# Performance work log

Measured on AMD Instinct MI355X. Metric: run time of the kernel, lower is better.

## Reference

```python
import jax, jax.numpy as jnp
import numpy as np

B, A, HR = 2, 180, 512
H_OUT = W_OUT = 512


def setup_inputs() -> dict:
    key = jax.random.key(0)
    k1, = jax.random.split(key, 1)
    sino = jax.random.normal(k1, (B, A, HR), dtype=jnp.float32)
    angles_deg = jnp.linspace(0.0, 180.0, A, endpoint=False, dtype=jnp.float32)
    return {"sino": sino, "angles_deg": angles_deg, "H": H_OUT, "W": W_OUT}


def _forward(sino, angles_deg, H, W):
    Bn, An, Hr = sino.shape
    pad = int(1.0 * 0.1 * min(H, W))  # pad_ratio = 1.0
    Hp, Wp = H + 2 * pad, W + 2 * pad

    # --- F.interpolate bilinear, align_corners=False: (A,B,Hr,1) -> (A,B,Hp,Wp).
    # Input width is 1, so width interp replicates the single column; only height interp matters.
    src = jnp.clip((jnp.arange(Hp, dtype=jnp.float32) + 0.5) * (Hr / Hp) - 0.5, 0.0, Hr - 1)
    i0 = jnp.floor(src).astype(jnp.int32)
    i1 = jnp.minimum(i0 + 1, Hr - 1)
    wH = src - i0.astype(jnp.float32)
    p = jnp.transpose(sino, (1, 0, 2)).astype(jnp.float32)  # (A,B,Hr)
    col = p[:, :, i0] * (1.0 - wH) + p[:, :, i1] * wH       # (A,B,Hp)
    proj = jnp.broadcast_to(col[:, :, :, None], (An, Bn, Hp, Wp))  # (A,B,Hp,Wp)

    # --- affine_grid (align_corners=False), sign = -1
    th = -jnp.deg2rad(angles_deg)
    c, s = jnp.cos(th), jnp.sin(th)                          # (A,)
    xs = (jnp.arange(Wp, dtype=jnp.float32) + 0.5) * (2.0 / Wp) - 1.0
    ys = (jnp.arange(Hp, dtype=jnp.float32) + 0.5) * (2.0 / Hp) - 1.0
    gx = c[:, None, None] * xs[None, None, :] - s[:, None, None] * ys[None, :, None]  # (A,Hp,Wp)
    gy = s[:, None, None] * xs[None, None, :] + c[:, None, None] * ys[None, :, None]

    # --- grid_sample bilinear, zeros padding, align_corners=False
    ix = ((gx + 1.0) * Wp - 1.0) * 0.5
    iy = ((gy + 1.0) * Hp - 1.0) * 0.5
    x0 = jnp.floor(ix).astype(jnp.int32); x1 = x0 + 1
    y0 = jnp.floor(iy).astype(jnp.int32); y1 = y0 + 1
    wx = ix - x0.astype(jnp.float32)
    wy = iy - y0.astype(jnp.float32)

    def corner(img, xi, yi, w):  # img (B,Hp,Wp); idx/w (Hp,Wp)
        valid = (xi >= 0) & (xi <= Wp - 1) & (yi >= 0) & (yi <= Hp - 1)
        xc = jnp.clip(xi, 0, Wp - 1)
        yc = jnp.clip(yi, 0, Hp - 1)
        return img[:, yc, xc] * (w * valid.astype(jnp.float32))[None]

    def sample(img, x0a, x1a, y0a, y1a, wxa, wya):
        return (corner(img, x0a, y0a, (1 - wxa) * (1 - wya)) +
                corner(img, x1a, y0a, wxa * (1 - wya)) +
                corner(img, x0a, y1a, (1 - wxa) * wya) +
                corner(img, x1a, y1a, wxa * wya))

    xr = jax.vmap(sample)(proj, x0, x1, y0, y1, wx, wy)      # (A,B,Hp,Wp)
    acc = xr.sum(axis=0) / (An + 1e-06)                      # (B,Hp,Wp)
    acc = acc[:, None, :, :]                                 # (B,1,Hp,Wp)
    if pad > 0:
        acc = acc[:, :, pad:Hp - pad, pad:Wp - pad]
    return acc


def reference(sino, angles_deg, H, W):
    return _forward(sino, angles_deg, H, W)
```

## Files before the change

kernel.cpp:

```cpp
#include <hip/hip_runtime.h>
#include <math.h>

#define B_N   2
#define A_N   180
#define HR_N  512
#define H_OUT 512
#define W_OUT 512
#define PAD   51
#define HP    614
#define WP    614
#define GUARD 80
#define HPP   (HP + 2*GUARD)
#define NPIX  (H_OUT * W_OUT)

#define TILE   16
#define CH     30
#define NCH    (A_N / CH)
#define WIN    24


__device__ __forceinline__ float col_val(const float* __restrict__ sino,
                                         int b, int a, int yy) {
    if (yy < 0 || yy >= HP) return 0.0f;
    float src = ((float)yy + 0.5f) * ((float)HR_N / (float)HP) - 0.5f;
    src = fminf(fmaxf(src, 0.0f), (float)(HR_N - 1));
    int i0 = (int)floorf(src);
    int i1 = min(i0 + 1, HR_N - 1);
    float wH = src - (float)i0;
    const float* srow = sino + ((size_t)b * A_N + a) * HR_N;
    return srow[i0] * (1.0f - wH) + srow[i1] * wH;
}

__global__ void prep_kernel(const float* __restrict__ sino,
                            const float* __restrict__ angles,
                            float4* __restrict__ pk,
                            float* __restrict__ tg) {
    int idx = blockIdx.x * blockDim.x + threadIdx.x;
    if (idx < A_N) {
        float th = -angles[idx] * (float)(M_PI / 180.0);
        tg[2 * idx]     = cosf(th);
        tg[2 * idx + 1] = sinf(th);
    }
    const int total = A_N * HPP;
    if (idx < total) {
        int y = idx % HPP;
        int a = idx / HPP;
        int yy = y - GUARD;
        float4 v;
        v.x = col_val(sino, 0, a, yy);
        v.y = col_val(sino, 1, a, yy);
        v.z = col_val(sino, 0, a, yy + 1);
        v.w = col_val(sino, 1, a, yy + 1);
        pk[idx] = v;
    }
}

__global__ __launch_bounds__(256) void bp_kernel(const float4* __restrict__ pk,
                                                 const float* __restrict__ tg,
                                                 float* __restrict__ out) {
    __shared__ float4 s_ang[A_N];
    __shared__ int    s_base[A_N];
    __shared__ float4 s_win[CH * WIN];

    int t  = threadIdx.x;
    int tx = blockIdx.x, ty = blockIdx.y;

    if (t < A_N) {
        float c = tg[2 * t];
        float s = tg[2 * t + 1];
        float Xc = (float)(tx * TILE) - 248.0f;
        float Yc = (float)(ty * TILE) - 248.0f;
        float iyc = fmaf(s, Xc, fmaf(c, Yc, 306.5f));
        int base = (int)floorf(iyc) - 11;
        s_ang[t]  = make_float4(c, s, (float)base, 0.0f);
        s_base[t] = base;
    }

    int lx = t & (TILE - 1);
    int ly = t >> 4;
    int w = tx * TILE + lx;
    int h = ty * TILE + ly;
    float X = (float)w - 255.5f;
    float Y = (float)h - 255.5f;

    float acc0 = 0.0f, acc1 = 0.0f;
    __syncthreads();

    for (int ch = 0; ch < NCH; ++ch) {
        int a0 = ch * CH;
        for (int e = t; e < CH * WIN; e += 256) {
            int la = e / WIN;
            int j  = e - la * WIN;
            int a  = a0 + la;
            int yy = s_base[a] + j + GUARD;
            s_win[e] = pk[(size_t)a * HPP + yy];
        }
        __syncthreads();

#pragma unroll 6
        for (int la = 0; la < CH; ++la) {
            float4 ang = s_ang[a0 + la];
            float c = ang.x, s = ang.y, fb = ang.z;
            float ix = fmaf(c, X, fmaf(-s, Y, 306.5f));
            float iy = fmaf(s, X, fmaf(c, Y, 306.5f));

            float xfac = fminf(fmaxf(ix + 1.0f, 0.0f), 1.0f)
                       * fminf(fmaxf((float)WP - ix, 0.0f), 1.0f);

            float f  = iy - fb;
            int   li = (int)f;
            float wy = f - (float)li;

            float4 cv = s_win[la * WIN + li];
            acc0 = fmaf(xfac, fmaf(wy, cv.z - cv.x, cv.x), acc0);
            acc1 = fmaf(xfac, fmaf(wy, cv.w - cv.y, cv.y), acc1);
        }
        __syncthreads();
    }

    const float inv = 1.0f / (180.0f + 1e-6f);
    int idx = h * W_OUT + w;
    out[idx]        = acc0 * inv;
    out[NPIX + idx] = acc1 * inv;
}

extern "C" void kernel_launch(void* const* d_in, const int* in_sizes, int n_in,
                              void* d_out, int out_size, void* d_ws, size_t ws_size,
                              hipStream_t stream) {
    const float* sino   = (const float*)d_in[0];
    const float* angles = (const float*)d_in[1];
    float* ws   = (float*)d_ws;
    float4* pk  = (float4*)ws;
    float* tg   = ws + (size_t)4 * A_N * HPP;

    const int total = A_N * HPP;
    prep_kernel<<<(total + 255) / 256, 256, 0, stream>>>(sino, angles, pk, tg);

    dim3 grid(W_OUT / TILE, H_OUT / TILE);
    bp_kernel<<<grid, 256, 0, stream>>>(pk, tg, (float*)d_out);
}
```

Before: 87.25 us.

## Pack projection table as fp16 and specialize interior tiles without x-bounds masking

Measured after the change: 91.38 us. 4.7% more time.

```diff
diff --git a/kernel.cpp b/kernel.cpp
--- a/kernel.cpp
+++ b/kernel.cpp
@@ -1,4 +1,5 @@
 #include <hip/hip_runtime.h>
+#include <hip/hip_fp16.h>
 #include <math.h>
 
 #define B_N   2
@@ -13,10 +14,10 @@
 #define HPP   (HP + 2*GUARD)
 #define NPIX  (H_OUT * W_OUT)
 
-#define TILE   16
-#define CH     30
-#define NCH    (A_N / CH)
-#define WIN    24
+#define TILE  16
+#define CH    30
+#define NCH   (A_N / CH)
+#define WIN   24
 
 
 __device__ __forceinline__ float col_val(const float* __restrict__ sino,
@@ -33,93 +34,115 @@
 
 __global__ void prep_kernel(const float* __restrict__ sino,
                             const float* __restrict__ angles,
-                            float4* __restrict__ pk,
-                            float* __restrict__ tg) {
+                            uint2* __restrict__ pk2,
+                            float2* __restrict__ tg) {
     int idx = blockIdx.x * blockDim.x + threadIdx.x;
     if (idx < A_N) {
         float th = -angles[idx] * (float)(M_PI / 180.0);
-        tg[2 * idx]     = cosf(th);
-        tg[2 * idx + 1] = sinf(th);
+        tg[idx] = make_float2(cosf(th), sinf(th));
     }
     const int total = A_N * HPP;
     if (idx < total) {
         int y = idx % HPP;
         int a = idx / HPP;
         int yy = y - GUARD;
-        float4 v;
-        v.x = col_val(sino, 0, a, yy);
-        v.y = col_val(sino, 1, a, yy);
-        v.z = col_val(sino, 0, a, yy + 1);
-        v.w = col_val(sino, 1, a, yy + 1);
-        pk[idx] = v;
+        float v00 = col_val(sino, 0, a, yy);
+        float v10 = col_val(sino, 1, a, yy);
+        float v01 = col_val(sino, 0, a, yy + 1);
+        float v11 = col_val(sino, 1, a, yy + 1);
+        __half2 lo = __floats2half2_rn(v00, v10);
+        __half2 hi = __floats2half2_rn(v01, v11);
+        uint2 u;
+        u.x = *(unsigned int*)&lo;
+        u.y = *(unsigned int*)&hi;
+        pk2[idx] = u;
     }
 }
 
-__global__ __launch_bounds__(256) void bp_kernel(const float4* __restrict__ pk,
-                                                 const float* __restrict__ tg,
-                                                 float* __restrict__ out) {
-    __shared__ float4 s_ang[A_N];
-    __shared__ int    s_base[A_N];
-    __shared__ float4 s_win[CH * WIN];
-
-    int t  = threadIdx.x;
-    int tx = blockIdx.x, ty = blockIdx.y;
-
-    if (t < A_N) {
-        float c = tg[2 * t];
-        float s = tg[2 * t + 1];
-        float Xc = (float)(tx * TILE) - 248.0f;
-        float Yc = (float)(ty * TILE) - 248.0f;
-        float iyc = fmaf(s, Xc, fmaf(c, Yc, 306.5f));
-        int base = (int)floorf(iyc) - 11;
-        s_ang[t]  = make_float4(c, s, (float)base, 0.0f);
-        s_base[t] = base;
-    }
-
-    int lx = t & (TILE - 1);
-    int ly = t >> 4;
-    int w = tx * TILE + lx;
-    int h = ty * TILE + ly;
-    float X = (float)w - 255.5f;
-    float Y = (float)h - 255.5f;
-
-    float acc0 = 0.0f, acc1 = 0.0f;
-    __syncthreads();
-
+template <bool INTERIOR>
+__device__ __forceinline__ void bp_body(const uint2* __restrict__ pk2,
+                                        const float2* __restrict__ tgv,
+                                        uint2* __restrict__ s_win,
+                                        const int* __restrict__ s_base,
+                                        int t, float X, float Y, float Xc, float Yc,
+                                        float& acc0, float& acc1) {
     for (int ch = 0; ch < NCH; ++ch) {
         int a0 = ch * CH;
         for (int e = t; e < CH * WIN; e += 256) {
             int la = e / WIN;
             int j  = e - la * WIN;
             int a  = a0 + la;
-            int yy = s_base[a] + j + GUARD;
-            s_win[e] = pk[(size_t)a * HPP + yy];
+            s_win[e] = pk2[(size_t)a * HPP + (GUARD + s_base[a] + j)];
         }
         __syncthreads();
 
 #pragma unroll 6
         for (int la = 0; la < CH; ++la) {
-            float4 ang = s_ang[a0 + la];
-            float c = ang.x, s = ang.y, fb = ang.z;
-            float ix = fmaf(c, X, fmaf(-s, Y, 306.5f));
-            float iy = fmaf(s, X, fmaf(c, Y, 306.5f));
-
-            float xfac = fminf(fmaxf(ix + 1.0f, 0.0f), 1.0f)
-                       * fminf(fmaxf((float)WP - ix, 0.0f), 1.0f);
-
-            float f  = iy - fb;
+            float2 cs = tgv[a0 + la];
+            float c = cs.x, s = cs.y;
+            float iyc   = fmaf(s, Xc, fmaf(c, Yc, 306.5f));
+            float basef = floorf(iyc);
+            float iyp   = fmaf(s, X, fmaf(c, Y, 317.5f));
+            float f  = iyp - basef;
             int   li = (int)f;
             float wy = f - (float)li;
 
-            float4 cv = s_win[la * WIN + li];
-            acc0 = fmaf(xfac, fmaf(wy, cv.z - cv.x, cv.x), acc0);
-            acc1 = fmaf(xfac, fmaf(wy, cv.w - cv.y, cv.y), acc1);
+            uint2 cv = s_win[la * WIN + li];
+            __half2 lo = *(__half2*)&cv.x;
+            __half2 hi = *(__half2*)&cv.y;
+            float c00 = __low2float(lo), c10 = __high2float(lo);
+            float c01 = __low2float(hi), c11 = __high2float(hi);
+
+            if (INTERIOR) {
+                acc0 = fmaf(wy, c01 - c00, acc0 + c00);
+                acc1 = fmaf(wy, c11 - c10, acc1 + c10);
+            } else {
+                float ix = fmaf(c, X, fmaf(-s, Y, 306.5f));
+                float xf = fminf(fmaxf(ix + 1.0f, 0.0f), 1.0f)
+                         * fminf(fmaxf((float)WP - ix, 0.0f), 1.0f);
+                float t0 = fmaf(wy, c01 - c00, c00);
+                float t1 = fmaf(wy, c11 - c10, c10);
+                acc0 = fmaf(xf, t0, acc0);
+                acc1 = fmaf(xf, t1, acc1);
+            }
         }
         __syncthreads();
     }
+}
+
+__global__ __launch_bounds__(256) void bp_kernel(const uint2* __restrict__ pk2,
+                                                 const float2* __restrict__ tgv,
+                                                 float* __restrict__ out) {
+    __shared__ uint2 s_win[CH * WIN];
+    __shared__ int   s_base[A_N];
+
+    int t  = threadIdx.x;
+    int tx = blockIdx.x, ty = blockIdx.y;
+    float Xc = (float)(tx * TILE) - 248.0f;
+    float Yc = (float)(ty * TILE) - 248.0f;
+
+    if (t < A_N) {
+        float2 cs = tgv[t];
+        float iyc = fmaf(cs.y, Xc, fmaf(cs.x, Yc, 306.5f));
+        s_base[t] = (int)floorf(iyc) - 11;
+    }
+
+    int lx = t & (TILE - 1);
+    int ly = t >> 4;
+    float X = (float)(tx * TILE + lx) - 255.5f;
+    float Y = (float)(ty * TILE + ly) - 255.5f;
+
+    float acc0 = 0.0f, acc1 = 0.0f;
+    __syncthreads();
+
+    bool interior = (Xc * Xc + Yc * Yc) <= 87500.0f;
+    if (interior)
+        bp_body<true >(pk2, tgv, s_win, s_base, t, X, Y, Xc, Yc, acc0, acc1);
+    else
+        bp_body<false>(pk2, tgv, s_win, s_base, t, X, Y, Xc, Yc, acc0, acc1);
 
     const float inv = 1.0f / (180.0f + 1e-6f);
-    int idx = h * W_OUT + w;
+    int idx = (ty * TILE + ly) * W_OUT + (tx * TILE + lx);
     out[idx]        = acc0 * inv;
     out[NPIX + idx] = acc1 * inv;
 }
@@ -129,13 +152,13 @@
                               hipStream_t stream) {
     const float* sino   = (const float*)d_in[0];
     const float* angles = (const float*)d_in[1];
-    float* ws   = (float*)d_ws;
-    float4* pk  = (float4*)ws;
-    float* tg   = ws + (size_t)4 * A_N * HPP;
+    char*   ws  = (char*)d_ws;
+    uint2*  pk2 = (uint2*)ws;
+    float2* tg  = (float2*)(ws + (size_t)A_N * HPP * sizeof(uint2));
 
     const int total = A_N * HPP;
-    prep_kernel<<<(total + 255) / 256, 256, 0, stream>>>(sino, angles, pk, tg);
+    prep_kernel<<<(total + 255) / 256, 256, 0, stream>>>(sino, angles, pk2, tg);
 
     dim3 grid(W_OUT / TILE, H_OUT / TILE);
-    bp_kernel<<<grid, 256, 0, stream>>>(pk, tg, (float*)d_out);
+    bp_kernel<<<grid, 256, 0, stream>>>(pk2, tg, (float*)d_out);
 }
```
